# Kernel optimization log

Measured on AMD Instinct MI355X. Metric: run time of the kernel, lower is better.

The kernel has to match this reference:

```python
import jax, jax.numpy as jnp
import numpy as np

B, S, H = 2, 2048, 2560
NH, NKV, D = 8, 4, 256
SW = 1024
EPS = 1e-6
NEG = -1e9


def _rms(x, w=None, eps=EPS):
    y = x * jax.lax.rsqrt(jnp.mean(x * x, axis=-1, keepdims=True) + eps)
    return y * (1.0 + w) if w is not None else y


def _rope(x, cos, sin):
    # x: [B, h, S, D]; cos/sin: [1, 1, S, D] with duplicated half-frequencies
    half = x.shape[-1] // 2
    out = x * cos
    o1 = out[..., :half] - x[..., half:] * sin[..., :half]
    o2 = out[..., half:] + x[..., :half] * sin[..., half:]
    return jnp.concatenate([o1, o2], axis=-1)


def setup_inputs() -> dict:
    key = jax.random.key(0)
    ks = jax.random.split(key, 6)
    hidden_states = jax.random.normal(ks[0], (B, S, H), dtype=jnp.float32)
    Wq = jax.random.normal(ks[1], (NH * D, H), dtype=jnp.float32) * 0.02
    Wk = jax.random.normal(ks[2], (NKV * D, H), dtype=jnp.float32) * 0.02
    Wv = jax.random.normal(ks[3], (NKV * D, H), dtype=jnp.float32) * 0.02
    Wo = jax.random.normal(ks[4], (H, NH * D), dtype=jnp.float32) * 0.02
    q_norm_w = jnp.zeros((D,), dtype=jnp.float32)
    k_norm_w = jnp.zeros((D,), dtype=jnp.float32)
    # RoPE tables (standard theta=10000, duplicated halves as in torch ref)
    pos = jnp.arange(S, dtype=jnp.float32)
    inv = 1.0 / (10000.0 ** (jnp.arange(0, D, 2, dtype=jnp.float32) / D))
    freqs = pos[:, None] * inv[None, :]            # [S, D/2]
    emb = jnp.concatenate([freqs, freqs], axis=-1)  # [S, D]
    cos = jnp.cos(emb)[None, None]                 # [1,1,S,D]
    sin = jnp.sin(emb)[None, None]
    # causal + sliding-window additive mask (allowed: i-SW < j <= i)
    i = jnp.arange(S)[:, None]
    j = jnp.arange(S)[None, :]
    allowed = (j <= i) & (j > i - SW)
    attention_mask = jnp.where(allowed, 0.0, NEG).astype(jnp.float32)[None, None]
    return {"hidden_states": hidden_states, "attention_mask": attention_mask,
            "cos": cos, "sin": sin, "Wq": Wq, "Wk": Wk, "Wv": Wv, "Wo": Wo,
            "q_norm_w": q_norm_w, "k_norm_w": k_norm_w}


def reference(hidden_states, attention_mask, cos, sin, Wq, Wk, Wv, Wo, q_norm_w, k_norm_w):
    b, s, _ = hidden_states.shape
    xq = (hidden_states @ Wq.T).reshape(b, s, NH, D).transpose(0, 2, 1, 3)  # [B,NH,S,D]
    xq = _rms(xq, q_norm_w)
    xk = (hidden_states @ Wk.T).reshape(b, s, NKV, D)
    xv = (hidden_states @ Wv.T).reshape(b, s, NKV, D)
    xk = _rms(xk, k_norm_w)
    xv = _rms(xv)  # parameterless rms_norm on v
    xk = xk.transpose(0, 2, 1, 3)  # [B,NKV,S,D]
    xv = xv.transpose(0, 2, 1, 3)
    xq = _rope(xq, cos, sin)
    xk = _rope(xk, cos, sin)
    # expand_kv path: S >= sliding_window and NH != NKV -> repeat_interleave
    g = NH // NKV
    xk = jnp.repeat(xk, g, axis=1)
    xv = jnp.repeat(xv, g, axis=1)
    # scale=1.0 in original (no 1/sqrt(d))
    scores = jnp.einsum('bhqd,bhkd->bhqk', xq, xk) + attention_mask
    attn = jax.nn.softmax(scores, axis=-1)
    out = jnp.einsum('bhqk,bhkd->bhqd', attn, xv)
    out = out.transpose(0, 2, 1, 3).reshape(b, s, NH * D)
    return out @ Wo.T
```

## Files before the change

kernel.cpp:

```cpp
#include <hip/hip_runtime.h>

#define B_   2
#define S_   2048
#define H_   2560
#define NH_  8
#define NKV_ 4
#define D_   256
#define SW_  1024

#define QKV_LD 4096

typedef __attribute__((ext_vector_type(8))) short    short8;
typedef __attribute__((ext_vector_type(8))) _Float16 half8;
typedef __attribute__((ext_vector_type(4))) _Float16 half4;
typedef __attribute__((ext_vector_type(4))) float    floatx4;
typedef __attribute__((ext_vector_type(2))) float    floatx2;

typedef unsigned int __attribute__((address_space(1))) as1_uint;
typedef unsigned int __attribute__((address_space(3))) as3_uint;

static __device__ __forceinline__ void async16(const void* g, void* l) {
    __builtin_amdgcn_global_load_lds((const as1_uint*)g, (as3_uint*)l, 16, 0, 0);
}

__global__ __launch_bounds__(256) void conv_all(
    const float* __restrict__ s0, const float* __restrict__ s1,
    const float* __restrict__ s2, const float* __restrict__ s3,
    const float* __restrict__ s4,
    _Float16* __restrict__ d0, _Float16* __restrict__ d1,
    _Float16* __restrict__ d2, _Float16* __restrict__ d3,
    _Float16* __restrict__ d4)
{
    const float* src; _Float16* dst; int n4;
    switch (blockIdx.y) {
        case 0:  src = s0; dst = d0; n4 = 4096 * 2560 / 4; break;
        case 1:  src = s1; dst = d1; n4 = 2048 * 2560 / 4; break;
        case 2:  src = s2; dst = d2; n4 = 1024 * 2560 / 4; break;
        case 3:  src = s3; dst = d3; n4 = 1024 * 2560 / 4; break;
        default: src = s4; dst = d4; n4 = 2560 * 2048 / 4; break;
    }
    for (int i = blockIdx.x * 256 + threadIdx.x; i < n4; i += gridDim.x * 256) {
        floatx4 v = *(const floatx4*)(src + (size_t)i * 4);
        half4 h = { (_Float16)v.x, (_Float16)v.y, (_Float16)v.z, (_Float16)v.w };
        *(half4*)(dst + (size_t)i * 4) = h;
    }
}

template <int C_FP32>
__global__ __launch_bounds__(256, 2) void gemm_f16(
    const _Float16* __restrict__ A,
    const _Float16* __restrict__ Bm,
    void* __restrict__ Cv,
    int M, int N, int K)
{
    __shared__ __align__(16) _Float16 As[128 * 32];
    __shared__ __align__(16) _Float16 Bs[128 * 32];

    const int tid  = threadIdx.x;
    const int lane = tid & 63, w = tid >> 6;
    const int wr = w >> 1, wc = w & 1;
    const int quad = lane >> 4, l16 = lane & 15;
    const int mBase = blockIdx.y * 128, nBase = blockIdx.x * 128;

    floatx4 acc[4][4];
    const floatx4 fzero = {0.f, 0.f, 0.f, 0.f};
#pragma unroll
    for (int i = 0; i < 4; ++i)
#pragma unroll
        for (int j = 0; j < 4; ++j) acc[i][j] = fzero;

    const int sRow = lane >> 2;
    const int sCol = (lane & 3) * 8;
    const size_t aRow = (size_t)(mBase + w * 32 + sRow);
    const size_t bRow = (size_t)(nBase + w * 32 + sRow);

    for (int kk = 0; kk < K; kk += 32) {
#pragma unroll
        for (int i = 0; i < 2; ++i) {
            async16(A  + (aRow + i * 16) * K + kk + sCol, &As[(w * 32 + i * 16) * 32]);
            async16(Bm + (bRow + i * 16) * K + kk + sCol, &Bs[(w * 32 + i * 16) * 32]);
        }
        __syncthreads();
        half8 af[4], bfv[4];
#pragma unroll
        for (int i = 0; i < 4; ++i)
            af[i] = *(const half8*)&As[(wr * 64 + i * 16 + l16) * 32 + quad * 8];
#pragma unroll
        for (int j = 0; j < 4; ++j)
            bfv[j] = *(const half8*)&Bs[(wc * 64 + j * 16 + l16) * 32 + quad * 8];
#pragma unroll
        for (int i = 0; i < 4; ++i)
#pragma unroll
            for (int j = 0; j < 4; ++j)
                acc[i][j] = __builtin_amdgcn_mfma_f32_16x16x32_f16(af[i], bfv[j], acc[i][j], 0, 0, 0);
        __syncthreads();
    }

#pragma unroll
    for (int i = 0; i < 4; ++i) {
        const int row0 = mBase + wr * 64 + i * 16 + quad * 4;
#pragma unroll
        for (int j = 0; j < 4; ++j) {
            const int col = nBase + wc * 64 + j * 16 + l16;
#pragma unroll
            for (int r = 0; r < 4; ++r) {
                const size_t idx = (size_t)(row0 + r) * N + col;
                if (C_FP32) ((float*)Cv)[idx] = acc[i][j][r];
                else        ((_Float16*)Cv)[idx] = (_Float16)acc[i][j][r];
            }
        }
    }
}

__global__ __launch_bounds__(256) void rmsrope_inplace(
    _Float16* __restrict__ qkv,
    const float* __restrict__ cosT,
    const float* __restrict__ sinT,
    const float* __restrict__ qw,
    const float* __restrict__ kw)
{
    const int t = blockIdx.x;
    const int s = t & (S_ - 1);
    const int tid = threadIdx.x, lane = tid & 63, w = tid >> 6;
    _Float16* row = qkv + (size_t)t * QKV_LD;
    const int d0 = lane * 2, d1 = 128 + lane * 2;

    floatx2 c0 = *(const floatx2*)(cosT + (size_t)s * D_ + d0);
    floatx2 c1 = *(const floatx2*)(cosT + (size_t)s * D_ + d1);
    floatx2 s0 = *(const floatx2*)(sinT + (size_t)s * D_ + d0);
    floatx2 s1 = *(const floatx2*)(sinT + (size_t)s * D_ + d1);
    floatx2 qw0 = *(const floatx2*)(qw + d0), qw1 = *(const floatx2*)(qw + d1);
    floatx2 kw0 = *(const floatx2*)(kw + d0), kw1 = *(const floatx2*)(kw + d1);

#pragma unroll
    for (int p = 0; p < 4; ++p) {
        const int v = w + p * 4;
        _Float16* x = row + v * D_;
        float x0a = (float)x[d0], x0b = (float)x[d0 + 1];
        float x1a = (float)x[d1], x1b = (float)x[d1 + 1];
        float ss = x0a * x0a + x0b * x0b + x1a * x1a + x1b * x1b;
#pragma unroll
        for (int off = 32; off > 0; off >>= 1) ss += __shfl_xor(ss, off, 64);
        const float rinv = rsqrtf(ss * (1.0f / 256.0f) + 1e-6f);
        if (v < 8) {
            const float y0a = x0a * rinv * (1.f + qw0.x), y0b = x0b * rinv * (1.f + qw0.y);
            const float y1a = x1a * rinv * (1.f + qw1.x), y1b = x1b * rinv * (1.f + qw1.y);
            x[d0] = (_Float16)(y0a * c0.x - y1a * s0.x);
            x[d0 + 1] = (_Float16)(y0b * c0.y - y1b * s0.y);
            x[d1] = (_Float16)(y1a * c1.x + y0a * s1.x);
            x[d1 + 1] = (_Float16)(y1b * c1.y + y0b * s1.y);
        } else if (v < 12) {
            const float y0a = x0a * rinv * (1.f + kw0.x), y0b = x0b * rinv * (1.f + kw0.y);
            const float y1a = x1a * rinv * (1.f + kw1.x), y1b = x1b * rinv * (1.f + kw1.y);
            x[d0] = (_Float16)(y0a * c0.x - y1a * s0.x);
            x[d0 + 1] = (_Float16)(y0b * c0.y - y1b * s0.y);
            x[d1] = (_Float16)(y1a * c1.x + y0a * s1.x);
            x[d1 + 1] = (_Float16)(y1b * c1.y + y0b * s1.y);
        } else {
            x[d0] = (_Float16)(x0a * rinv);
            x[d0 + 1] = (_Float16)(x0b * rinv);
            x[d1] = (_Float16)(x1a * rinv);
            x[d1 + 1] = (_Float16)(x1b * rinv);
        }
    }
}

__global__ __launch_bounds__(256) void transpose_v(
    const _Float16* __restrict__ qkv, _Float16* __restrict__ Vt)
{
    __shared__ _Float16 tile[64][66];
    const int s0 = blockIdx.x * 64;
    const int dd0 = blockIdx.y * 64;
    const int bk = blockIdx.z;
    const int b = bk >> 2, kvh = bk & 3;
    const _Float16* src = qkv + (size_t)(b * S_) * QKV_LD + 3072 + kvh * D_;
    _Float16* dst = Vt + (size_t)bk * D_ * S_;
    const int tx = threadIdx.x & 63, ty = threadIdx.x >> 6;
    for (int r = ty; r < 64; r += 4)
        tile[r][tx] = src[(size_t)(s0 + r) * QKV_LD + dd0 + tx];
    __syncthreads();
    for (int r = ty; r < 64; r += 4)
        dst[(size_t)(dd0 + r) * S_ + s0 + tx] = tile[tx][r];
}

#define PS_STRIDE 40

__global__ __launch_bounds__(256, 2) void attn_kernel(
    const _Float16* __restrict__ qkv,
    const _Float16* __restrict__ Vt,
    _Float16* __restrict__ Oa)
{
    __shared__ __align__(16) _Float16 Ks[2][32 * 256];
    __shared__ __align__(16) _Float16 Vs[2][256 * 32];
    __shared__ __align__(16) _Float16 Ps[4][16 * PS_STRIDE];

    const int qb = blockIdx.x * 64;
    const int h = blockIdx.y, b = blockIdx.z;
    const int kvh = h >> 1;
    const int tid = threadIdx.x, lane = tid & 63, w = tid >> 6;
    const int quad = lane >> 4, l16 = lane & 15;

    const _Float16* Qrow = qkv + ((size_t)(b * S_ + qb + w * 16 + l16)) * QKV_LD + h * D_;
    half8 qf[8];
#pragma unroll
    for (int kst = 0; kst < 8; ++kst)
        qf[kst] = *(const half8*)(Qrow + kst * 32 + quad * 8);

    floatx4 o[16];
    const floatx4 fzero = {0.f, 0.f, 0.f, 0.f};
#pragma unroll
    for (int dt = 0; dt < 16; ++dt) o[dt] = fzero;
    float mrow[4] = {-1e30f, -1e30f, -1e30f, -1e30f};
    float lrow[4] = {0.f, 0.f, 0.f, 0.f};

    const _Float16* Kbase  = qkv + (size_t)(b * S_) * QKV_LD + 2048 + kvh * D_;
    const _Float16* Vtbase = Vt + (size_t)(b * NKV_ + kvh) * D_ * S_;
    const int kb_start = (qb >= SW_) ? qb - SW_ : 0;
    const int kb_end = qb + 32;

    auto stage = [&](int kb, int bufi) {
#pragma unroll
        for (int p = 0; p < 4; ++p) {
            const int keyl = w * 8 + p * 2 + (lane >> 5);
            const int g = ((lane & 31) - keyl) & 31;
            async16(Kbase + (size_t)(kb + keyl) * QKV_LD + g * 8,
                    &Ks[bufi][(w * 8 + p * 2) * 256]);
        }
#pragma unroll
        for (int p = 0; p < 4; ++p) {
            const int drow = w * 64 + p * 16 + (lane >> 2);
            const int q = lane & 3;
            async16(Vtbase + (size_t)drow * S_ + kb + q * 8,
                    &Vs[bufi][(w * 64 + p * 16) * 32]);
        }
    };

    int buf = 0;
    stage(kb_start, 0);

    for (int kb = kb_start; kb <= kb_end; kb += 32) {
        __syncthreads();
        if (kb + 32 <= kb_end) stage(kb + 32, buf ^ 1);

        floatx4 sacc[2];
        sacc[0] = fzero; sacc[1] = fzero;
#pragma unroll
        for (int jt = 0; jt < 2; ++jt) {
            const int keyl = jt * 16 + l16;
#pragma unroll
            for (int kst = 0; kst < 8; ++kst) {
                const int crot = (kst * 4 + quad + keyl) & 31;
                half8 kf = *(const half8*)&Ks[buf][keyl * 256 + crot * 8];
                sacc[jt] = __builtin_amdgcn_mfma_f32_16x16x32_f16(qf[kst], kf, sacc[jt], 0, 0, 0);
            }
        }

        const int q0 = qb + w * 16 + quad * 4;
        float sval[2][4], tmax[4];
#pragma unroll
        for (int r = 0; r < 4; ++r) tmax[r] = -1e30f;
#pragma unroll
        for (int jt = 0; jt < 2; ++jt) {
            const int kg = kb + jt * 16 + l16;
#pragma unroll
            for (int r = 0; r < 4; ++r) {
                const int qg = q0 + r;
                const bool ok = (kg <= qg) && (kg + SW_ > qg);
                const float vv = ok ? sacc[jt][r] : -1e30f;
                sval[jt][r] = vv;
                tmax[r] = fmaxf(tmax[r], vv);
            }
        }
#pragma unroll
        for (int r = 0; r < 4; ++r) {
#pragma unroll
            for (int off = 1; off < 16; off <<= 1)
                tmax[r] = fmaxf(tmax[r], __shfl_xor(tmax[r], off, 64));
            const float mnew = fmaxf(mrow[r], tmax[r]);
            const float alpha = __expf(mrow[r] - mnew);
            mrow[r] = mnew;
            lrow[r] *= alpha;
            tmax[r] = alpha;
        }
        float rsum[4] = {0.f, 0.f, 0.f, 0.f};
#pragma unroll
        for (int jt = 0; jt < 2; ++jt)
#pragma unroll
            for (int r = 0; r < 4; ++r) {
                float pv = __expf(sval[jt][r] - mrow[r]);
                pv = (sval[jt][r] <= -1e29f) ? 0.0f : pv;
                rsum[r] += pv;
                Ps[w][(quad * 4 + r) * PS_STRIDE + jt * 16 + l16] = (_Float16)pv;
            }
#pragma unroll
        for (int r = 0; r < 4; ++r) {
#pragma unroll
            for (int off = 1; off < 16; off <<= 1)
                rsum[r] += __shfl_xor(rsum[r], off, 64);
            lrow[r] += rsum[r];
        }
#pragma unroll
        for (int dt = 0; dt < 16; ++dt)
#pragma unroll
            for (int r = 0; r < 4; ++r) o[dt][r] *= tmax[r];

        half8 pa = *(const half8*)&Ps[w][l16 * PS_STRIDE + quad * 8];
#pragma unroll
        for (int dt = 0; dt < 16; ++dt) {
            half8 vf = *(const half8*)&Vs[buf][(dt * 16 + l16) * 32 + quad * 8];
            o[dt] = __builtin_amdgcn_mfma_f32_16x16x32_f16(pa, vf, o[dt], 0, 0, 0);
        }
        buf ^= 1;
    }

    const int qrow = qb + w * 16 + quad * 4;
#pragma unroll
    for (int r = 0; r < 4; ++r) {
        const float inv = (lrow[r] > 0.f) ? (1.0f / lrow[r]) : 0.f;
        _Float16* orow = Oa + ((size_t)(b * S_ + qrow + r)) * (NH_ * D_) + h * D_;
#pragma unroll
        for (int dt = 0; dt < 16; ++dt)
            orow[dt * 16 + l16] = (_Float16)(o[dt][r] * inv);
    }
}

extern "C" void kernel_launch(void* const* d_in, const int* in_sizes, int n_in,
                              void* d_out, int out_size, void* d_ws, size_t ws_size,
                              hipStream_t stream)
{
    (void)in_sizes; (void)n_in; (void)out_size; (void)ws_size;
    const float* hid  = (const float*)d_in[0];
    const float* cosT = (const float*)d_in[2];
    const float* sinT = (const float*)d_in[3];
    const float* Wq   = (const float*)d_in[4];
    const float* Wk   = (const float*)d_in[5];
    const float* Wv   = (const float*)d_in[6];
    const float* Wo   = (const float*)d_in[7];
    const float* qw   = (const float*)d_in[8];
    const float* kw   = (const float*)d_in[9];
    float* out = (float*)d_out;

    char* ws = (char*)d_ws;
    _Float16* qkv  = (_Float16*)(ws);
    _Float16* attn = (_Float16*)(ws + 33554432ull);
    _Float16* hidH = (_Float16*)(ws + 50331648ull);
    _Float16* wQKV = (_Float16*)(ws + 71303168ull);
    _Float16* woH  = (_Float16*)(ws + 92274688ull);
    _Float16* Vt   = (_Float16*)(ws + 102760448ull);

    conv_all<<<dim3(512, 5), 256, 0, stream>>>(
        hid, Wq, Wk, Wv, Wo,
        hidH, wQKV, wQKV + (size_t)2048 * 2560, wQKV + (size_t)3072 * 2560, woH);

    gemm_f16<0><<<dim3(32, 32), 256, 0, stream>>>(hidH, wQKV, qkv, 4096, 4096, 2560);
    rmsrope_inplace<<<4096, 256, 0, stream>>>(qkv, cosT, sinT, qw, kw);
    transpose_v<<<dim3(32, 4, 8), 256, 0, stream>>>(qkv, Vt);
    attn_kernel<<<dim3(32, 8, 2), 256, 0, stream>>>(qkv, Vt, attn);
    gemm_f16<1><<<dim3(20, 32), 256, 0, stream>>>(attn, woH, out, 4096, 2560, 2048);
}
```

Baseline: 435.3 us.

## Replace GEMM with 256x256-tile double-buffered pipelined MFMA kernel

Both projection GEMMs now use a new kernel with 512 threads and 256x256 output tiles over a 64-wide K step. A and B tiles are double-buffered in LDS with XOR-swizzled layouts, and the next tiles are loaded asynchronously while MFMAs run, using explicit waitcnt, barriers and setprio. Block indices are swizzled across XCDs to improve L2 reuse. This raises arithmetic intensity and hides load latency, but uses about 128KB of LDS per block. The output projection also drops to 160 blocks, which may leave CUs idle.

```diff
diff --git a/kernel.cpp b/kernel.cpp
--- a/kernel.cpp
+++ b/kernel.cpp
@@ -47,66 +47,141 @@
 }
 
 template <int C_FP32>
-__global__ __launch_bounds__(256, 2) void gemm_f16(
+__global__ __launch_bounds__(512, 2) void gemm256(
     const _Float16* __restrict__ A,
     const _Float16* __restrict__ Bm,
     void* __restrict__ Cv,
-    int M, int N, int K)
-{
-    __shared__ __align__(16) _Float16 As[128 * 32];
-    __shared__ __align__(16) _Float16 Bs[128 * 32];
+    int M, int N, int K, int NBX)
+{
+    (void)M;
+    __shared__ __align__(16) _Float16 As[2][256 * 64];
+    __shared__ __align__(16) _Float16 Bs[2][256 * 64];
 
     const int tid  = threadIdx.x;
     const int lane = tid & 63, w = tid >> 6;
-    const int wr = w >> 1, wc = w & 1;
+    const int wr = w >> 2, wc = w & 3;
     const int quad = lane >> 4, l16 = lane & 15;
-    const int mBase = blockIdx.y * 128, nBase = blockIdx.x * 128;
-
-    floatx4 acc[4][4];
-    const floatx4 fzero = {0.f, 0.f, 0.f, 0.f};
-#pragma unroll
-    for (int i = 0; i < 4; ++i)
-#pragma unroll
-        for (int j = 0; j < 4; ++j) acc[i][j] = fzero;
-
-    const int sRow = lane >> 2;
-    const int sCol = (lane & 3) * 8;
-    const size_t aRow = (size_t)(mBase + w * 32 + sRow);
-    const size_t bRow = (size_t)(nBase + w * 32 + sRow);
-
-    for (int kk = 0; kk < K; kk += 32) {
-#pragma unroll
-        for (int i = 0; i < 2; ++i) {
-            async16(A  + (aRow + i * 16) * K + kk + sCol, &As[(w * 32 + i * 16) * 32]);
-            async16(Bm + (bRow + i * 16) * K + kk + sCol, &Bs[(w * 32 + i * 16) * 32]);
-        }
-        __syncthreads();
-        half8 af[4], bfv[4];
-#pragma unroll
-        for (int i = 0; i < 4; ++i)
-            af[i] = *(const half8*)&As[(wr * 64 + i * 16 + l16) * 32 + quad * 8];
-#pragma unroll
-        for (int j = 0; j < 4; ++j)
-            bfv[j] = *(const half8*)&Bs[(wc * 64 + j * 16 + l16) * 32 + quad * 8];
-#pragma unroll
-        for (int i = 0; i < 4; ++i)
-#pragma unroll
-            for (int j = 0; j < 4; ++j)
-                acc[i][j] = __builtin_amdgcn_mfma_f32_16x16x32_f16(af[i], bfv[j], acc[i][j], 0, 0, 0);
-        __syncthreads();
-    }
-
-#pragma unroll
-    for (int i = 0; i < 4; ++i) {
-        const int row0 = mBase + wr * 64 + i * 16 + quad * 4;
-#pragma unroll
-        for (int j = 0; j < 4; ++j) {
-            const int col = nBase + wc * 64 + j * 16 + l16;
+
+    const int nwg = gridDim.x, cpx = nwg >> 3;
+    const int swz = (blockIdx.x & 7) * cpx + (blockIdx.x >> 3);
+    const int mBase = (swz / NBX) * 256, nBase = (swz % NBX) * 256;
+
+    const int NT = K >> 6;
+
+    const int stRow = w * 8 + (lane >> 3);
+    const int stCol = (((lane & 7) ^ (lane >> 3)) << 3);
+    const int rdsw  = (l16 & 7) << 3;
+
+    const _Float16* Ag = A  + (size_t)mBase * K;
+    const _Float16* Bg = Bm + (size_t)nBase * K;
+
+    floatx4 acc[8][4];
+    const floatx4 fz = {0.f, 0.f, 0.f, 0.f};
+#pragma unroll
+    for (int i = 0; i < 8; ++i)
+#pragma unroll
+        for (int j = 0; j < 4; ++j) acc[i][j] = fz;
+
+    auto stA = [&](int tt, int h, _Float16* dst) {
+#pragma unroll
+        for (int r = 0; r < 2; ++r) {
+            const int rb = h * 128 + r * 64;
+            async16(Ag + (size_t)(rb + stRow) * K + tt * 64 + stCol,
+                    dst + (size_t)(rb + w * 8) * 64);
+        }
+    };
+    auto stB = [&](int tt, int h, _Float16* dst) {
+#pragma unroll
+        for (int r = 0; r < 2; ++r) {
+            const int rb = h * 128 + r * 64;
+            async16(Bg + (size_t)(rb + stRow) * K + tt * 64 + stCol,
+                    dst + (size_t)(rb + w * 8) * 64);
+        }
+    };
+
+    stA(0, 0, &As[0][0]); stA(0, 1, &As[0][0]);
+    stB(0, 0, &Bs[0][0]); stB(0, 1, &Bs[0][0]);
+    if (NT > 1) { stB(1, 0, &Bs[1][0]); stB(1, 1, &Bs[1][0]); }
+    asm volatile("s_waitcnt vmcnt(4)" ::: "memory");
+    __builtin_amdgcn_s_barrier();
+
+    auto tile = [&](int t, _Float16* Ab, _Float16* Bb, _Float16* Ao) {
+        half8 bf[4][2], af[2][2];
+#pragma unroll
+        for (int c = 0; c < 4; ++c) {
+            const int brow = wc * 64 + c * 16 + l16;
+#pragma unroll
+            for (int s = 0; s < 2; ++s)
+                bf[c][s] = *(const half8*)&Bb[(size_t)brow * 64 + ((s * 32 + quad * 8) ^ rdsw)];
+        }
+#pragma unroll
+        for (int r = 0; r < 2; ++r) {
+            const int arow = wr * 128 + r * 16 + l16;
+#pragma unroll
+            for (int s = 0; s < 2; ++s)
+                af[r][s] = *(const half8*)&Ab[(size_t)arow * 64 + ((s * 32 + quad * 8) ^ rdsw)];
+        }
+        if (t + 1 < NT) stA(t + 1, 0, Ao);
+        asm volatile("s_waitcnt lgkmcnt(8)");
+        __builtin_amdgcn_s_barrier();
+        asm volatile("s_waitcnt lgkmcnt(0)");
+        __builtin_amdgcn_s_setprio(1);
+#pragma unroll
+        for (int s = 0; s < 2; ++s)
+#pragma unroll
+            for (int c = 0; c < 4; ++c) {
+                acc[0][c] = __builtin_amdgcn_mfma_f32_16x16x32_f16(af[0][s], bf[c][s], acc[0][c], 0, 0, 0);
+                acc[1][c] = __builtin_amdgcn_mfma_f32_16x16x32_f16(af[1][s], bf[c][s], acc[1][c], 0, 0, 0);
+            }
+        __builtin_amdgcn_s_setprio(0);
+        __builtin_amdgcn_s_barrier();
+#pragma unroll
+        for (int p = 1; p < 4; ++p) {
+#pragma unroll
+            for (int r = 0; r < 2; ++r) {
+                const int arow = wr * 128 + (2 * p + r) * 16 + l16;
+#pragma unroll
+                for (int s = 0; s < 2; ++s)
+                    af[r][s] = *(const half8*)&Ab[(size_t)arow * 64 + ((s * 32 + quad * 8) ^ rdsw)];
+            }
+            if (p == 1)      { if (t + 1 < NT) stA(t + 1, 1, Ao); }
+            else if (p == 2) { if (t + 2 < NT) stB(t + 2, 0, Bb); }
+            else             { if (t + 2 < NT) stB(t + 2, 1, Bb); }
+            __builtin_amdgcn_s_barrier();
+            asm volatile("s_waitcnt lgkmcnt(0)");
+            __builtin_amdgcn_s_setprio(1);
+#pragma unroll
+            for (int s = 0; s < 2; ++s)
+#pragma unroll
+                for (int c = 0; c < 4; ++c) {
+                    acc[2 * p][c]     = __builtin_amdgcn_mfma_f32_16x16x32_f16(af[0][s], bf[c][s], acc[2 * p][c], 0, 0, 0);
+                    acc[2 * p + 1][c] = __builtin_amdgcn_mfma_f32_16x16x32_f16(af[1][s], bf[c][s], acc[2 * p + 1][c], 0, 0, 0);
+                }
+            __builtin_amdgcn_s_setprio(0);
+            if (p == 3) {
+                if (t < NT - 2) asm volatile("s_waitcnt vmcnt(4)" ::: "memory");
+                else            asm volatile("s_waitcnt vmcnt(0)" ::: "memory");
+            }
+            __builtin_amdgcn_s_barrier();
+        }
+    };
+
+    for (int t = 0; t < NT; t += 2) {
+        tile(t,     &As[0][0], &Bs[0][0], &As[1][0]);
+        tile(t + 1, &As[1][0], &Bs[1][0], &As[0][0]);
+    }
+
+#pragma unroll
+    for (int fr = 0; fr < 8; ++fr) {
+        const int row0 = mBase + wr * 128 + fr * 16 + quad * 4;
+#pragma unroll
+        for (int c = 0; c < 4; ++c) {
+            const int col = nBase + wc * 64 + c * 16 + l16;
 #pragma unroll
             for (int r = 0; r < 4; ++r) {
                 const size_t idx = (size_t)(row0 + r) * N + col;
-                if (C_FP32) ((float*)Cv)[idx] = acc[i][j][r];
-                else        ((_Float16*)Cv)[idx] = (_Float16)acc[i][j][r];
+                if (C_FP32) ((float*)Cv)[idx] = acc[fr][c][r];
+                else        ((_Float16*)Cv)[idx] = (_Float16)acc[fr][c][r];
             }
         }
     }
@@ -352,9 +427,9 @@
         hid, Wq, Wk, Wv, Wo,
         hidH, wQKV, wQKV + (size_t)2048 * 2560, wQKV + (size_t)3072 * 2560, woH);
 
-    gemm_f16<0><<<dim3(32, 32), 256, 0, stream>>>(hidH, wQKV, qkv, 4096, 4096, 2560);
+    gemm256<0><<<dim3(256), 512, 0, stream>>>(hidH, wQKV, qkv, 4096, 4096, 2560, 16);
     rmsrope_inplace<<<4096, 256, 0, stream>>>(qkv, cosT, sinT, qw, kw);
     transpose_v<<<dim3(32, 4, 8), 256, 0, stream>>>(qkv, Vt);
     attn_kernel<<<dim3(32, 8, 2), 256, 0, stream>>>(qkv, Vt, attn);
-    gemm_f16<1><<<dim3(20, 32), 256, 0, stream>>>(attn, woH, out, 4096, 2560, 2048);
-}
+    gemm256<1><<<dim3(160), 512, 0, stream>>>(attn, woH, out, 4096, 2560, 2048, 10);
+}
```

Result: faster. 415.6 us (-4.5%).
